# Kernel optimization log

Hardware: AMD Instinct MI355X
Metric: run time of the kernel (lower is better)

## Reference

```python
import jax, jax.numpy as jnp
import numpy as np

N, E = 50000, 600000
IN, H, C = 128, 8, 32
HC = H * C
LAT, OUT, NCOM = 32, 64, 30
BN_EPS = 1e-5
NEG_SLOPE = 0.2


def setup_inputs() -> dict:
    key = jax.random.key(0)
    ks = jax.random.split(key, 32)
    f32 = jnp.float32
    def rn(i, shape, s=0.05):
        return jax.random.normal(ks[i], shape, f32) * s
    inp = {
        'x': jax.random.normal(ks[0], (N, IN), f32),
        'eps': jax.random.normal(ks[1], (N, LAT), f32),
        'edge_index': jax.random.randint(ks[2], (2, E), 0, N, jnp.int32),
        # GAT layer 1 (in -> H*C)
        'gat1_W': rn(3, (IN, HC)), 'gat1_asrc': rn(4, (H, C)), 'gat1_adst': rn(5, (H, C)), 'gat1_b': jnp.zeros((HC,), f32),
        'bn1_g': jnp.ones((HC,), f32), 'bn1_b': jnp.zeros((HC,), f32),
        # GAT layer 2 (H*C -> H*C)
        'gat2_W': rn(6, (HC, HC)), 'gat2_asrc': rn(7, (H, C)), 'gat2_adst': rn(8, (H, C)), 'gat2_b': jnp.zeros((HC,), f32),
        'bn2_g': jnp.ones((HC,), f32), 'bn2_b': jnp.zeros((HC,), f32),
        # GAT layer 3 (H*C -> H*C)
        'gat3_W': rn(9, (HC, HC)), 'gat3_asrc': rn(10, (H, C)), 'gat3_adst': rn(11, (H, C)), 'gat3_b': jnp.zeros((HC,), f32),
        'bn3_g': jnp.ones((HC,), f32), 'bn3_b': jnp.zeros((HC,), f32),
        # heads
        'res_W': rn(12, (IN, HC)), 'res_b': jnp.zeros((HC,), f32),
        'mu_W': rn(13, (HC, LAT)), 'mu_b': jnp.zeros((LAT,), f32),
        'lv_W': rn(14, (HC, LAT)), 'lv_b': jnp.zeros((LAT,), f32),
        'dec_W': rn(15, (LAT, OUT)), 'dec_b': jnp.zeros((OUT,), f32),
        'aux_W': rn(16, (HC, NCOM)), 'aux_b': jnp.zeros((NCOM,), f32),
    }
    return inp


def gat_conv(x, src, dst, W, asrc, adst, b):
    # PyG GATConv (concat=True, self-loops already in src/dst, lin bias=False)
    n = x.shape[0]
    h = (x @ W).reshape(n, H, C)                      # [N,H,C]
    a_s = jnp.einsum('nhc,hc->nh', h, asrc)           # [N,H]
    a_d = jnp.einsum('nhc,hc->nh', h, adst)
    e = jax.nn.leaky_relu(a_s[src] + a_d[dst], NEG_SLOPE)  # [E,H]
    m = jax.ops.segment_max(e, dst, num_segments=n)        # per-dest softmax (stable)
    p = jnp.exp(e - m[dst])
    s = jax.ops.segment_sum(p, dst, num_segments=n)
    alpha = p / (s[dst] + 1e-16)                      # [E,H]
    out = jax.ops.segment_sum(h[src] * alpha[:, :, None], dst, num_segments=n)
    return out.reshape(n, HC) + b


def batch_norm(x, g, b):
    mu = x.mean(0)
    var = x.var(0)  # biased var, as torch BN uses for normalization
    return (x - mu) * jax.lax.rsqrt(var + BN_EPS) * g + b


def reference(x, eps, edge_index,
              gat1_W, gat1_asrc, gat1_adst, gat1_b, bn1_g, bn1_b,
              gat2_W, gat2_asrc, gat2_adst, gat2_b, bn2_g, bn2_b,
              gat3_W, gat3_asrc, gat3_adst, gat3_b, bn3_g, bn3_b,
              res_W, res_b, mu_W, mu_b, lv_W, lv_b, dec_W, dec_b, aux_W, aux_b):
    loops = jnp.arange(N, dtype=edge_index.dtype)
    src = jnp.concatenate([edge_index[0], loops])
    dst = jnp.concatenate([edge_index[1], loops])

    residual = x @ res_W + res_b
    h = jax.nn.relu(batch_norm(gat_conv(x, src, dst, gat1_W, gat1_asrc, gat1_adst, gat1_b), bn1_g, bn1_b))
    h = jax.nn.relu(batch_norm(gat_conv(h, src, dst, gat2_W, gat2_asrc, gat2_adst, gat2_b), bn2_g, bn2_b))
    h = jax.nn.relu(batch_norm(gat_conv(h, src, dst, gat3_W, gat3_asrc, gat3_adst, gat3_b), bn3_g, bn3_b))
    h = h + residual

    mu = h @ mu_W + mu_b
    logvar = h @ lv_W + lv_b
    z = mu + eps * jnp.exp(0.5 * logvar)   # reparameterize
    out = z @ dec_W + dec_b
    aux = h @ aux_W + aux_b
    return (out, mu, logvar, aux)
```

## Files before the change

kernel.cpp:

```cpp
#include <hip/hip_runtime.h>

#define N_NODES 50000
#define N_EDGES 600000
#define HC 256
#define NH 8
#define AGG_BLOCKS 2048
#define AGG_WAVES (AGG_BLOCKS * 4)

typedef short s8v __attribute__((ext_vector_type(8)));
typedef float f4v __attribute__((ext_vector_type(4)));
typedef _Float16 h4v __attribute__((ext_vector_type(4)));
typedef _Float16 h8v __attribute__((ext_vector_type(8)));
typedef __attribute__((address_space(1))) const unsigned int as1_cu32;
typedef __attribute__((address_space(3))) unsigned int as3_u32;

__device__ inline ushort f2bf(float f) {
  unsigned u = __float_as_uint(f);
  unsigned r = u + 0x7FFF + ((u >> 16) & 1);
  return (ushort)(r >> 16);
}

__global__ void k_init_cnt(int* __restrict__ cnt) {
  int i = blockIdx.x * 256 + threadIdx.x;
  if (i < N_NODES) cnt[i] = 1;
}

__global__ void k_count(const int* __restrict__ dstE, int* __restrict__ cnt) {
  int e = blockIdx.x * 256 + threadIdx.x;
  if (e < N_EDGES) atomicAdd(&cnt[dstE[e]], 1);
}

__global__ void k_scan_bsum(const int* __restrict__ cnt, int* __restrict__ bsum) {
  __shared__ int sd[256];
  int i = blockIdx.x * 256 + threadIdx.x;
  sd[threadIdx.x] = (i < N_NODES) ? cnt[i] : 0;
  __syncthreads();
  for (int o = 128; o > 0; o >>= 1) {
    if (threadIdx.x < o) sd[threadIdx.x] += sd[threadIdx.x + o];
    __syncthreads();
  }
  if (threadIdx.x == 0) bsum[blockIdx.x] = sd[0];
}

__global__ void k_scan_offsets(int* __restrict__ bsum, int nb) {
  __shared__ int s[256];
  int t = threadIdx.x;
  int v = (t < nb) ? bsum[t] : 0;
  s[t] = v; __syncthreads();
  for (int o = 1; o < 256; o <<= 1) {
    int x = (t >= o) ? s[t - o] : 0;
    __syncthreads();
    s[t] += x;
    __syncthreads();
  }
  if (t < nb) bsum[t] = s[t] - v;
}

__global__ void k_scan_write(const int* __restrict__ cnt, const int* __restrict__ bsum,
                             int* __restrict__ rowptr, int* __restrict__ fillptr) {
  __shared__ int s[256];
  int t = threadIdx.x;
  int i = blockIdx.x * 256 + t;
  int v = (i < N_NODES) ? cnt[i] : 0;
  s[t] = v; __syncthreads();
  for (int o = 1; o < 256; o <<= 1) {
    int x = (t >= o) ? s[t - o] : 0;
    __syncthreads();
    s[t] += x;
    __syncthreads();
  }
  int excl = s[t] - v + bsum[blockIdx.x];
  if (i < N_NODES) {
    rowptr[i] = excl;
    fillptr[i] = excl;
    if (i == N_NODES - 1) rowptr[N_NODES] = excl + v;
  }
}

__global__ void k_fill(const int* __restrict__ srcE, const int* __restrict__ dstE,
                       int* __restrict__ fillptr, int* __restrict__ srcs) {
  int i = blockIdx.x * 256 + threadIdx.x;
  if (i < N_NODES) {
    int pos = atomicAdd(&fillptr[i], 1);
    srcs[pos] = i;
  } else if (i < N_NODES + N_EDGES) {
    int e = i - N_NODES;
    int pos = atomicAdd(&fillptr[dstE[e]], 1);
    srcs[pos] = srcE[e];
  }
}

__global__ void k_cvt_x(const float* __restrict__ X, ushort* __restrict__ Xb) {
  size_t i = ((size_t)blockIdx.x * 256 + threadIdx.x) * 4;
  float4 x4 = *(const float4*)&X[i];
  ushort4 o;
  o.x = f2bf(x4.x); o.y = f2bf(x4.y); o.z = f2bf(x4.z); o.w = f2bf(x4.w);
  *(ushort4*)&Xb[i] = o;
}

__global__ void k_prep(const float* __restrict__ gW0, const float* __restrict__ resW,
                       const float* __restrict__ gW1, const float* __restrict__ gW2,
                       const float* __restrict__ muW, const float* __restrict__ lvW,
                       const float* __restrict__ auxW,
                       ushort* __restrict__ WtP, ushort* __restrict__ Wt2,
                       ushort* __restrict__ Wt3, ushort* __restrict__ Wth) {
  __shared__ ushort s[32][33];
  int id = blockIdx.x;
  int t = threadIdx.x;
  if (id < 64) {
    const float* W = (id < 32) ? gW0 : resW;
    ushort* Wt = (id < 32) ? WtP : (WtP + 256 * 128);
    int a = id & 31;
    int bx = a & 3, by = a >> 2;
    int tx = t & 31, ty = t >> 5;
    int k0 = bx * 32, n0 = by * 32;
    for (int j = 0; j < 32; j += 8)
      s[ty + j][tx] = f2bf(W[(size_t)(k0 + ty + j) * 256 + n0 + tx]);
    __syncthreads();
    for (int j = 0; j < 32; j += 8)
      Wt[(size_t)(n0 + ty + j) * 128 + k0 + tx] = s[tx][ty + j];
  } else if (id < 192) {
    const float* W = (id < 128) ? gW1 : gW2;
    ushort* Wt = (id < 128) ? Wt2 : Wt3;
    int a = (id - 64) & 63;
    int bx = a & 7, by = a >> 3;
    int tx = t & 31, ty = t >> 5;
    int k0 = bx * 32, n0 = by * 32;
    for (int j = 0; j < 32; j += 8)
      s[ty + j][tx] = f2bf(W[(size_t)(k0 + ty + j) * 256 + n0 + tx]);
    __syncthreads();
    for (int j = 0; j < 32; j += 8)
      Wt[(size_t)(n0 + ty + j) * 256 + k0 + tx] = s[tx][ty + j];
  } else {
    int n = id - 192;
    int k = t;
    float v = 0.f;
    if (n < 32) v = muW[k * 32 + n];
    else if (n < 64) v = lvW[k * 32 + (n - 32)];
    else if (n < 94) v = auxW[k * 30 + (n - 64)];
    Wth[n * 256 + k] = f2bf(v);
  }
}

template <typename OutT>
__launch_bounds__(256)
__global__ void k_gemm_bf16(const ushort* __restrict__ A, const ushort* __restrict__ Wt,
                            const float* __restrict__ bias, int bias_off, OutT* __restrict__ Out,
                            int M, int K, int ldc,
                            const float* __restrict__ att_asrc, const float* __restrict__ att_adst,
                            float* __restrict__ att_as, float* __restrict__ att_ad) {
  __shared__ __align__(16) ushort As[16 * 512];
  __shared__ __align__(16) ushort Bs[8 * 512];
  int t = threadIdx.x, w = t >> 6, L = t & 63;
  int bm = blockIdx.x * 128, bn = blockIdx.y * 64;
  int lrow = L & 15, lcol = (L >> 4) * 8;

  const ushort* ga[4];
  const ushort* gb[2];
#pragma unroll
  for (int u = 0; u < 4; u++) {
    int i = w * 4 + u;
    int mt = i >> 1, ks = i & 1;
    int arow = bm + mt * 16 + lrow;
    if (arow >= M) arow = M - 1;
    ga[u] = A + (size_t)arow * K + ks * 32 + lcol;
  }
#pragma unroll
  for (int u = 0; u < 2; u++) {
    int i = w * 2 + u;
    int mt = i >> 1, ks = i & 1;
    int brow = bn + mt * 16 + lrow;
    gb[u] = Wt + (size_t)brow * K + ks * 32 + lcol;
  }

  f4v acc[4][2];
  f4v zero = {0.f, 0.f, 0.f, 0.f};
#pragma unroll
  for (int mi = 0; mi < 4; mi++)
#pragma unroll
    for (int ni = 0; ni < 2; ni++) acc[mi][ni] = zero;

  int wm = (w >> 1) * 4;
  int wn = (w & 1) * 2;

  int nk = K >> 6;
  for (int kt = 0; kt < nk; kt++) {
#pragma unroll
    for (int u = 0; u < 4; u++) {
      int i = w * 4 + u;
      __builtin_amdgcn_global_load_lds((as1_cu32*)ga[u], (as3_u32*)&As[i * 512], 16, 0, 0);
      ga[u] += 64;
    }
#pragma unroll
    for (int u = 0; u < 2; u++) {
      int i = w * 2 + u;
      __builtin_amdgcn_global_load_lds((as1_cu32*)gb[u], (as3_u32*)&Bs[i * 512], 16, 0, 0);
      gb[u] += 64;
    }
    __syncthreads();
#pragma unroll
    for (int ks = 0; ks < 2; ks++) {
      s8v af[4], bf[2];
#pragma unroll
      for (int mi = 0; mi < 4; mi++)
        af[mi] = *(const s8v*)&As[(((wm + mi) * 2 + ks) * 64 + L) * 8];
#pragma unroll
      for (int ni = 0; ni < 2; ni++)
        bf[ni] = *(const s8v*)&Bs[(((wn + ni) * 2 + ks) * 64 + L) * 8];
#pragma unroll
      for (int mi = 0; mi < 4; mi++)
#pragma unroll
        for (int ni = 0; ni < 2; ni++)
          acc[mi][ni] = __builtin_amdgcn_mfma_f32_16x16x32_bf16(af[mi], bf[ni], acc[mi][ni], 0, 0, 0);
    }
    __syncthreads();
  }
#pragma unroll
  for (int ni = 0; ni < 2; ni++) {
    int col = bn + (wn + ni) * 16 + (L & 15);
    float bb = (bias && col >= bias_off) ? bias[col - bias_off] : 0.f;
#pragma unroll
    for (int mi = 0; mi < 4; mi++) {
      int rbase = bm + (wm + mi) * 16 + (L >> 4) * 4;
#pragma unroll
      for (int i = 0; i < 4; i++) {
        int r = rbase + i;
        if (r < M) Out[(size_t)r * ldc + col] = (OutT)(acc[mi][ni][i] + bb);
      }
    }
  }
  if (att_as && bn < 256) {
    int hb = ((unsigned)(bn + wn * 16)) >> 5;
    int cl = L & 15;
    float sa0 = att_asrc[hb * 32 + cl],  sa1 = att_asrc[hb * 32 + 16 + cl];
    float da0 = att_adst[hb * 32 + cl],  da1 = att_adst[hb * 32 + 16 + cl];
#pragma unroll
    for (int mi = 0; mi < 4; mi++) {
#pragma unroll
      for (int i = 0; i < 4; i++) {
        float vs = acc[mi][0][i] * sa0 + acc[mi][1][i] * sa1;
        float vd = acc[mi][0][i] * da0 + acc[mi][1][i] * da1;
        vs += __shfl_xor(vs, 1); vd += __shfl_xor(vd, 1);
        vs += __shfl_xor(vs, 2); vd += __shfl_xor(vd, 2);
        vs += __shfl_xor(vs, 4); vd += __shfl_xor(vd, 4);
        vs += __shfl_xor(vs, 8); vd += __shfl_xor(vd, 8);
        int r = bm + (wm + mi) * 16 + (L >> 4) * 4 + i;
        if (cl == 0 && r < M) {
          att_as[r * NH + hb] = vs;
          att_ad[r * NH + hb] = vd;
        }
      }
    }
  }
}

__launch_bounds__(256)
__global__ void k_gemm_head(const ushort* __restrict__ A, const ushort* __restrict__ Wt,
                            const float* __restrict__ eps,
                            const float* __restrict__ mub, const float* __restrict__ lvb,
                            const float* __restrict__ auxb,
                            const float* __restrict__ decW, const float* __restrict__ decb,
                            float* __restrict__ out) {
  __shared__ __align__(16) ushort smem[16384];
  __shared__ float wsd[2048];
  __shared__ float shz[4][32];
  ushort* As = smem;
  ushort* Bs = smem + 8192;
  int t = threadIdx.x, w = t >> 6, L = t & 63;
  int bm = blockIdx.x * 128;
  int lrow = L & 15, lcol = (L >> 4) * 8;
  const int K = 256;
  for (int i = t; i < 2048; i += 256) wsd[i] = decW[i];

  const ushort* ga[4];
  const ushort* gb[4];
#pragma unroll
  for (int u = 0; u < 4; u++) {
    int i = w * 4 + u;
    int mt = i >> 1, ks = i & 1;
    int arow = bm + mt * 16 + lrow;
    if (arow >= N_NODES) arow = N_NODES - 1;
    ga[u] = A + (size_t)arow * K + ks * 32 + lcol;
    int brow = mt * 16 + lrow;
    gb[u] = Wt + (size_t)brow * K + ks * 32 + lcol;
  }
  f4v acc[4][4];
  f4v zero = {0.f, 0.f, 0.f, 0.f};
#pragma unroll
  for (int mi = 0; mi < 4; mi++)
#pragma unroll
    for (int ni = 0; ni < 4; ni++) acc[mi][ni] = zero;
  int wm = (w >> 1) * 4;
  int wn = (w & 1) * 4;
  for (int kt = 0; kt < 4; kt++) {
#pragma unroll
    for (int u = 0; u < 4; u++) {
      int i = w * 4 + u;
      __builtin_amdgcn_global_load_lds((as1_cu32*)ga[u], (as3_u32*)&As[i * 512], 16, 0, 0);
      __builtin_amdgcn_global_load_lds((as1_cu32*)gb[u], (as3_u32*)&Bs[i * 512], 16, 0, 0);
      ga[u] += 64; gb[u] += 64;
    }
    __syncthreads();
#pragma unroll
    for (int ks = 0; ks < 2; ks++) {
      s8v af[4], bf[4];
#pragma unroll
      for (int mi = 0; mi < 4; mi++)
        af[mi] = *(const s8v*)&As[(((wm + mi) * 2 + ks) * 64 + L) * 8];
#pragma unroll
      for (int ni = 0; ni < 4; ni++)
        bf[ni] = *(const s8v*)&Bs[(((wn + ni) * 2 + ks) * 64 + L) * 8];
#pragma unroll
      for (int mi = 0; mi < 4; mi++)
#pragma unroll
        for (int ni = 0; ni < 4; ni++)
          acc[mi][ni] = __builtin_amdgcn_mfma_f32_16x16x32_bf16(af[mi], bf[ni], acc[mi][ni], 0, 0, 0);
    }
    __syncthreads();
  }
  _Float16* tile = (_Float16*)smem;
#pragma unroll
  for (int ni = 0; ni < 4; ni++) {
    int c = (wn + ni) * 16 + (L & 15);
#pragma unroll
    for (int mi = 0; mi < 4; mi++) {
      int rbase = (wm + mi) * 16 + (L >> 4) * 4;
#pragma unroll
      for (int i = 0; i < 4; i++)
        tile[(rbase + i) * 128 + c] = (_Float16)acc[mi][ni][i];
    }
  }
  __syncthreads();
  for (int rr = 0; rr < 32; rr++) {
    int rl = w * 32 + rr;
    int n = bm + rl;
    bool valid = n < N_NODES;
    if (L < 32) {
      float mu = (float)tile[rl * 128 + L] + mub[L];
      float lv = (float)tile[rl * 128 + 32 + L] + lvb[L];
      float zv = 0.f;
      if (valid) {
        out[(size_t)N_NODES * 64 + (size_t)n * 32 + L] = mu;
        out[(size_t)N_NODES * 96 + (size_t)n * 32 + L] = lv;
        zv = mu + eps[(size_t)n * 32 + L] * __expf(0.5f * lv);
      }
      shz[w][L] = zv;
    } else if (L < 62 && valid) {
      int j = L - 32;
      out[(size_t)N_NODES * 128 + (size_t)n * 30 + j] = (float)tile[rl * 128 + 64 + j] + auxb[j];
    }
    __syncthreads();
    float o = decb[L];
#pragma unroll 8
    for (int kk = 0; kk < 32; kk++) o += shz[w][kk] * wsd[kk * 64 + L];
    if (valid) out[(size_t)n * 64 + L] = o;
    __syncthreads();
  }
}

#define FMA4(P, B2)                                                                        \
  asm("v_fma_mix_f32 %0, %1, %2, %0 op_sel:[0,0,0] op_sel_hi:[0,1,0]"                      \
      : "+v"(ac0) : "v"(P), "v"((B2).x));                                                  \
  asm("v_fma_mix_f32 %0, %1, %2, %0 op_sel:[0,1,0] op_sel_hi:[0,1,0]"                      \
      : "+v"(ac1) : "v"(P), "v"((B2).x));                                                  \
  asm("v_fma_mix_f32 %0, %1, %2, %0 op_sel:[0,0,0] op_sel_hi:[0,1,0]"                      \
      : "+v"(ac2) : "v"(P), "v"((B2).y));                                                  \
  asm("v_fma_mix_f32 %0, %1, %2, %0 op_sel:[0,1,0] op_sel_hi:[0,1,0]"                      \
      : "+v"(ac3) : "v"(P), "v"((B2).y));

__launch_bounds__(256)
__global__ void k_agg(const int* __restrict__ rowptr, const int* __restrict__ srcs,
                      const float* __restrict__ as_, const float* __restrict__ ad_,
                      const _Float16* __restrict__ B, int ld, const float* __restrict__ gb,
                      _Float16* __restrict__ C, float* __restrict__ part,
                      float* __restrict__ stats) {
  __shared__ float ss[4 * 512];
  int t = threadIdx.x;
  if (blockIdx.x == 0) {
    stats[t] = 0.f; stats[t + 256] = 0.f;
  }
  int w = t >> 6, lane = t & 63;
  int h = lane >> 3;
  int cb = lane << 2;
  int ldu = ld >> 2;
  const uint2* Bu = (const uint2*)B;
  float4 g4 = *(const float4*)&gb[cb];
  float sts0 = 0.f, sts1 = 0.f, sts2 = 0.f, sts3 = 0.f;
  float stq0 = 0.f, stq1 = 0.f, stq2 = 0.f, stq3 = 0.f;

  for (int n = blockIdx.x * 4 + w; n < N_NODES; n += AGG_WAVES) {
    int beg = rowptr[n], end = rowptr[n + 1];
    float ad_nh = ad_[n * NH + h];
    float ac0 = 0.f, ac1 = 0.f, ac2 = 0.f, ac3 = 0.f, wsum = 0.f;
    int k = beg;
    for (; k + 4 <= end; k += 4) {
      int s0 = srcs[k], s1 = srcs[k + 1], s2 = srcs[k + 2], s3 = srcs[k + 3];
      uint2 b0 = Bu[(size_t)s0 * ldu + lane];
      uint2 b1 = Bu[(size_t)s1 * ldu + lane];
      uint2 b2 = Bu[(size_t)s2 * ldu + lane];
      uint2 b3 = Bu[(size_t)s3 * ldu + lane];
      float e0 = as_[s0 * NH + h] + ad_nh; e0 = e0 > 0.f ? e0 : 0.2f * e0;
      float e1 = as_[s1 * NH + h] + ad_nh; e1 = e1 > 0.f ? e1 : 0.2f * e1;
      float e2 = as_[s2 * NH + h] + ad_nh; e2 = e2 > 0.f ? e2 : 0.2f * e2;
      float e3 = as_[s3 * NH + h] + ad_nh; e3 = e3 > 0.f ? e3 : 0.2f * e3;
      float p0 = __expf(e0), p1 = __expf(e1), p2 = __expf(e2), p3 = __expf(e3);
      wsum += (p0 + p1) + (p2 + p3);
      FMA4(p0, b0)
      FMA4(p1, b1)
      FMA4(p2, b2)
      FMA4(p3, b3)
    }
    for (; k < end; k++) {
      int s = srcs[k];
      h4v b4 = *(const h4v*)&B[(size_t)s * ld + cb];
      float e = as_[s * NH + h] + ad_nh;
      e = e > 0.f ? e : 0.2f * e;
      float p = __expf(e);
      wsum += p;
      ac0 += p * (float)b4[0]; ac1 += p * (float)b4[1];
      ac2 += p * (float)b4[2]; ac3 += p * (float)b4[3];
    }
    float inv = 1.f / (wsum + 1e-16f);
    float v0 = ac0 * inv + g4.x, v1 = ac1 * inv + g4.y;
    float v2 = ac2 * inv + g4.z, v3 = ac3 * inv + g4.w;
    h4v o; o[0] = (_Float16)v0; o[1] = (_Float16)v1; o[2] = (_Float16)v2; o[3] = (_Float16)v3;
    *(h4v*)&C[(size_t)n * 256 + cb] = o;
    sts0 += v0; stq0 += v0 * v0;
    sts1 += v1; stq1 += v1 * v1;
    sts2 += v2; stq2 += v2 * v2;
    sts3 += v3; stq3 += v3 * v3;
  }
  float* sw = &ss[w * 512];
  sw[cb + 0] = sts0; sw[cb + 1] = sts1; sw[cb + 2] = sts2; sw[cb + 3] = sts3;
  sw[256 + cb + 0] = stq0; sw[256 + cb + 1] = stq1;
  sw[256 + cb + 2] = stq2; sw[256 + cb + 3] = stq3;
  __syncthreads();
  float p0 = ss[t] + ss[512 + t] + ss[1024 + t] + ss[1536 + t];
  float p1 = ss[256 + t] + ss[768 + t] + ss[1280 + t] + ss[1792 + t];
  part[(size_t)blockIdx.x * 512 + t] = p0;
  part[(size_t)blockIdx.x * 512 + 256 + t] = p1;
}

__global__ void k_bn_reduce(const float* __restrict__ part, float* __restrict__ stats) {
  int i = threadIdx.x;
  int base = blockIdx.x * (AGG_BLOCKS / 16);
  float s0 = 0.f, s1 = 0.f;
  for (int b = 0; b < AGG_BLOCKS / 16; b++) {
    s0 += part[(size_t)(base + b) * 512 + i];
    s1 += part[(size_t)(base + b) * 512 + 256 + i];
  }
  atomicAdd(&stats[i], s0);
  atomicAdd(&stats[256 + i], s1);
}

__global__ void k_bn_relu_cvt(const _Float16* __restrict__ X, const float* __restrict__ stats,
                              const float* __restrict__ g, const float* __restrict__ b,
                              const _Float16* __restrict__ resid, int rld,
                              ushort* __restrict__ Xb) {
  size_t i = ((size_t)blockIdx.x * 256 + threadIdx.x) * 8;
  int c = (int)(i & 255);
  const float invN = 1.f / (float)N_NODES;
  h8v x8 = *(const h8v*)&X[i];
  float v[8];
#pragma unroll
  for (int q = 0; q < 2; q++) {
    float4 s4 = *(const float4*)&stats[c + q * 4];
    float4 q4 = *(const float4*)&stats[256 + c + q * 4];
    float4 g4 = *(const float4*)&g[c + q * 4];
    float4 b4 = *(const float4*)&b[c + q * 4];
    float m0 = s4.x * invN, m1 = s4.y * invN, m2 = s4.z * invN, m3 = s4.w * invN;
    v[q * 4 + 0] = ((float)x8[q * 4 + 0] - m0) * rsqrtf(q4.x * invN - m0 * m0 + 1e-5f) * g4.x + b4.x;
    v[q * 4 + 1] = ((float)x8[q * 4 + 1] - m1) * rsqrtf(q4.y * invN - m1 * m1 + 1e-5f) * g4.y + b4.y;
    v[q * 4 + 2] = ((float)x8[q * 4 + 2] - m2) * rsqrtf(q4.z * invN - m2 * m2 + 1e-5f) * g4.z + b4.z;
    v[q * 4 + 3] = ((float)x8[q * 4 + 3] - m3) * rsqrtf(q4.w * invN - m3 * m3 + 1e-5f) * g4.w + b4.w;
  }
#pragma unroll
  for (int q = 0; q < 8; q++) v[q] = v[q] > 0.f ? v[q] : 0.f;
  if (resid) {
    size_t row = i >> 8;
    h8v r8 = *(const h8v*)&resid[row * rld + c];
#pragma unroll
    for (int q = 0; q < 8; q++) v[q] += (float)r8[q];
  }
  ushort o8[8];
#pragma unroll
  for (int q = 0; q < 8; q++) o8[q] = f2bf(v[q]);
  *(uint4*)&Xb[i] = *(const uint4*)o8;
}

extern "C" void kernel_launch(void* const* d_in, const int* in_sizes, int n_in,
                              void* d_out, int out_size, void* d_ws, size_t ws_size,
                              hipStream_t stream) {
  (void)in_sizes; (void)n_in; (void)out_size; (void)ws_size;
  const float* x    = (const float*)d_in[0];
  const float* eps  = (const float*)d_in[1];
  const int*   ei   = (const int*)d_in[2];
  const float* gW[3]    = {(const float*)d_in[3],  (const float*)d_in[9],  (const float*)d_in[15]};
  const float* gasrc[3] = {(const float*)d_in[4],  (const float*)d_in[10], (const float*)d_in[16]};
  const float* gadst[3] = {(const float*)d_in[5],  (const float*)d_in[11], (const float*)d_in[17]};
  const float* gbias[3] = {(const float*)d_in[6],  (const float*)d_in[12], (const float*)d_in[18]};
  const float* bng[3]   = {(const float*)d_in[7],  (const float*)d_in[13], (const float*)d_in[19]};
  const float* bnb[3]   = {(const float*)d_in[8],  (const float*)d_in[14], (const float*)d_in[20]};
  const float* resW = (const float*)d_in[21];
  const float* resb = (const float*)d_in[22];
  const float* muW  = (const float*)d_in[23];
  const float* mub  = (const float*)d_in[24];
  const float* lvW  = (const float*)d_in[25];
  const float* lvb  = (const float*)d_in[26];
  const float* decW = (const float*)d_in[27];
  const float* decb = (const float*)d_in[28];
  const float* auxW = (const float*)d_in[29];
  const float* auxb = (const float*)d_in[30];
  float* out = (float*)d_out;

  char* ws = (char*)d_ws;
  size_t off = 0;
  auto alloc = [&](size_t bytes) -> void* {
    void* p = ws + off;
    off += (bytes + 255) & ~(size_t)255;
    return p;
  };
  _Float16* X0R = (_Float16*)alloc((size_t)N_NODES * 512 * 2);
  _Float16* X0  = (_Float16*)alloc((size_t)N_NODES * HC * 2);
  _Float16* X1  = (_Float16*)alloc((size_t)N_NODES * HC * 2);
  ushort* Xb    = (ushort*)alloc((size_t)N_NODES * HC * 2);
  float*  as_   = (float*)alloc((size_t)N_NODES * NH * 4);
  float*  ad_   = (float*)alloc((size_t)N_NODES * NH * 4);
  float*  stats = (float*)alloc(512 * 4);
  float*  part  = (float*)alloc((size_t)AGG_BLOCKS * 512 * 4);
  int* cnt      = (int*)alloc((size_t)N_NODES * 4);
  int* rowptr   = (int*)alloc((size_t)(N_NODES + 1) * 4);
  int* fillptr  = (int*)alloc((size_t)N_NODES * 4);
  int* srcs     = (int*)alloc((size_t)(N_NODES + N_EDGES) * 4);
  int* bsum     = (int*)alloc(256 * 4);
  ushort* WtP   = (ushort*)alloc(512 * 128 * 2);
  ushort* Wt2   = (ushort*)alloc(256 * 256 * 2);
  ushort* Wt3   = (ushort*)alloc(256 * 256 * 2);
  ushort* Wth   = (ushort*)alloc(128 * 256 * 2);

  const int NB = (N_NODES + 255) / 256;
  k_init_cnt<<<NB, 256, 0, stream>>>(cnt);
  k_count<<<(N_EDGES + 255) / 256, 256, 0, stream>>>(ei + N_EDGES, cnt);
  k_scan_bsum<<<NB, 256, 0, stream>>>(cnt, bsum);
  k_scan_offsets<<<1, 256, 0, stream>>>(bsum, NB);
  k_scan_write<<<NB, 256, 0, stream>>>(cnt, bsum, rowptr, fillptr);
  k_fill<<<(N_NODES + N_EDGES + 255) / 256, 256, 0, stream>>>(ei, ei + N_EDGES, fillptr, srcs);

  k_prep<<<320, 256, 0, stream>>>(gW[0], resW, gW[1], gW[2], muW, lvW, auxW, WtP, Wt2, Wt3, Wth);
  k_cvt_x<<<(N_NODES * 128) / 1024, 256, 0, stream>>>(x, Xb);

  const int GM = (N_NODES + 127) / 128;
  const int EW_GRID = (N_NODES * HC) / 2048;

  k_gemm_bf16<_Float16><<<dim3(GM, 8), 256, 0, stream>>>(
      Xb, WtP, resb, 256, X0R, N_NODES, 128, 512, gasrc[0], gadst[0], as_, ad_);
  k_agg<<<AGG_BLOCKS, 256, 0, stream>>>(rowptr, srcs, as_, ad_, X0R, 512, gbias[0], X1, part, stats);
  k_bn_reduce<<<16, 256, 0, stream>>>(part, stats);
  k_bn_relu_cvt<<<EW_GRID, 256, 0, stream>>>(X1, stats, bng[0], bnb[0], nullptr, 0, Xb);

  const ushort* Wts[2] = {Wt2, Wt3};
  for (int L = 0; L < 2; L++) {
    k_gemm_bf16<_Float16><<<dim3(GM, 4), 256, 0, stream>>>(
        Xb, Wts[L], nullptr, 0, X0, N_NODES, 256, 256, gasrc[L + 1], gadst[L + 1], as_, ad_);
    k_agg<<<AGG_BLOCKS, 256, 0, stream>>>(rowptr, srcs, as_, ad_, X0, 256, gbias[L + 1], X1, part, stats);
    k_bn_reduce<<<16, 256, 0, stream>>>(part, stats);
    k_bn_relu_cvt<<<EW_GRID, 256, 0, stream>>>(
        X1, stats, bng[L + 1], bnb[L + 1], (L == 1) ? (X0R + 256) : nullptr, 512, Xb);
  }
  k_gemm_head<<<GM, 256, 0, stream>>>(Xb, Wth, eps, mub, lvb, auxb, decW, decb, out);
}
```

Before: 608.2 us.

## Fuse batch-norm, ReLU and residual into next GEMM's A-tile load

Removes the standalone BN+ReLU+bf16 conversion kernel by applying normalization, ReLU and (for the final layer) residual addition while staging the A tile in the following GEMM and head kernels. This avoids a full write and re-read of the intermediate activation buffer and several launches. In exchange, A tiles are loaded synchronously through registers instead of via async global-to-LDS copies, and each row is re-normalized once per column block of the GEMM grid.

```diff
diff --git a/kernel.cpp b/kernel.cpp
--- a/kernel.cpp
+++ b/kernel.cpp
@@ -255,7 +255,140 @@
 }
 
 __launch_bounds__(256)
-__global__ void k_gemm_head(const ushort* __restrict__ A, const ushort* __restrict__ Wt,
+__global__ void k_gemm_bn(const _Float16* __restrict__ A, const ushort* __restrict__ Wt,
+                          const float* __restrict__ stats, const float* __restrict__ g,
+                          const float* __restrict__ b, _Float16* __restrict__ Out,
+                          const float* __restrict__ att_asrc, const float* __restrict__ att_adst,
+                          float* __restrict__ att_as, float* __restrict__ att_ad) {
+  __shared__ __align__(16) ushort As[16 * 512];
+  __shared__ __align__(16) ushort Bs[8 * 512];
+  const int K = 256, M = N_NODES, ldc = 256;
+  const float invN = 1.f / (float)N_NODES;
+  int t = threadIdx.x, w = t >> 6, L = t & 63;
+  int bm = blockIdx.x * 128, bn = blockIdx.y * 64;
+  int lrow = L & 15, lcol = (L >> 4) * 8;
+
+  int arow[4];
+  const ushort* gb[2];
+#pragma unroll
+  for (int u = 0; u < 4; u++) {
+    int i = w * 4 + u;
+    int mt = i >> 1;
+    int r = bm + mt * 16 + lrow;
+    arow[u] = (r >= M) ? (M - 1) : r;
+  }
+#pragma unroll
+  for (int u = 0; u < 2; u++) {
+    int i = w * 2 + u;
+    int mt = i >> 1, ks = i & 1;
+    gb[u] = Wt + (size_t)(bn + mt * 16 + lrow) * K + ks * 32 + lcol;
+  }
+
+  f4v acc[4][2];
+  f4v zero = {0.f, 0.f, 0.f, 0.f};
+#pragma unroll
+  for (int mi = 0; mi < 4; mi++)
+#pragma unroll
+    for (int ni = 0; ni < 2; ni++) acc[mi][ni] = zero;
+
+  int wm = (w >> 1) * 4;
+  int wn = (w & 1) * 2;
+
+  for (int kt = 0; kt < 4; kt++) {
+#pragma unroll
+    for (int u = 0; u < 2; u++) {
+      int i = w * 2 + u;
+      __builtin_amdgcn_global_load_lds((as1_cu32*)gb[u], (as3_u32*)&Bs[i * 512], 16, 0, 0);
+      gb[u] += 64;
+    }
+#pragma unroll
+    for (int u = 0; u < 4; u++) {
+      int i = w * 4 + u;
+      int ks = i & 1;
+      int c0 = kt * 64 + ks * 32 + lcol;
+      h8v a8 = *(const h8v*)&A[(size_t)arow[u] * 256 + c0];
+      ushort o8[8];
+#pragma unroll
+      for (int q2 = 0; q2 < 2; q2++) {
+        float4 s4 = *(const float4*)&stats[c0 + q2 * 4];
+        float4 q4 = *(const float4*)&stats[256 + c0 + q2 * 4];
+        float4 g4 = *(const float4*)&g[c0 + q2 * 4];
+        float4 b4 = *(const float4*)&b[c0 + q2 * 4];
+        float sm[4] = {s4.x, s4.y, s4.z, s4.w};
+        float qm[4] = {q4.x, q4.y, q4.z, q4.w};
+        float gm[4] = {g4.x, g4.y, g4.z, g4.w};
+        float bm_[4] = {b4.x, b4.y, b4.z, b4.w};
+#pragma unroll
+        for (int j = 0; j < 4; j++) {
+          float m = sm[j] * invN;
+          float rs = rsqrtf(qm[j] * invN - m * m + 1e-5f) * gm[j];
+          float v = ((float)a8[q2 * 4 + j] - m) * rs + bm_[j];
+          v = v > 0.f ? v : 0.f;
+          o8[q2 * 4 + j] = f2bf(v);
+        }
+      }
+      *(uint4*)&As[(size_t)i * 512 + L * 8] = *(const uint4*)o8;
+    }
+    __syncthreads();
+#pragma unroll
+    for (int ks = 0; ks < 2; ks++) {
+      s8v af[4], bf[2];
+#pragma unroll
+      for (int mi = 0; mi < 4; mi++)
+        af[mi] = *(const s8v*)&As[(((wm + mi) * 2 + ks) * 64 + L) * 8];
+#pragma unroll
+      for (int ni = 0; ni < 2; ni++)
+        bf[ni] = *(const s8v*)&Bs[(((wn + ni) * 2 + ks) * 64 + L) * 8];
+#pragma unroll
+      for (int mi = 0; mi < 4; mi++)
+#pragma unroll
+        for (int ni = 0; ni < 2; ni++)
+          acc[mi][ni] = __builtin_amdgcn_mfma_f32_16x16x32_bf16(af[mi], bf[ni], acc[mi][ni], 0, 0, 0);
+    }
+    __syncthreads();
+  }
+#pragma unroll
+  for (int ni = 0; ni < 2; ni++) {
+    int col = bn + (wn + ni) * 16 + (L & 15);
+#pragma unroll
+    for (int mi = 0; mi < 4; mi++) {
+      int rbase = bm + (wm + mi) * 16 + (L >> 4) * 4;
+#pragma unroll
+      for (int i = 0; i < 4; i++) {
+        int r = rbase + i;
+        if (r < M) Out[(size_t)r * ldc + col] = (_Float16)(acc[mi][ni][i]);
+      }
+    }
+  }
+  {
+    int hb = ((unsigned)(bn + wn * 16)) >> 5;
+    int cl = L & 15;
+    float sa0 = att_asrc[hb * 32 + cl],  sa1 = att_asrc[hb * 32 + 16 + cl];
+    float da0 = att_adst[hb * 32 + cl],  da1 = att_adst[hb * 32 + 16 + cl];
+#pragma unroll
+    for (int mi = 0; mi < 4; mi++) {
+#pragma unroll
+      for (int i = 0; i < 4; i++) {
+        float vs = acc[mi][0][i] * sa0 + acc[mi][1][i] * sa1;
+        float vd = acc[mi][0][i] * da0 + acc[mi][1][i] * da1;
+        vs += __shfl_xor(vs, 1); vd += __shfl_xor(vd, 1);
+        vs += __shfl_xor(vs, 2); vd += __shfl_xor(vd, 2);
+        vs += __shfl_xor(vs, 4); vd += __shfl_xor(vd, 4);
+        vs += __shfl_xor(vs, 8); vd += __shfl_xor(vd, 8);
+        int r = bm + (wm + mi) * 16 + (L >> 4) * 4 + i;
+        if (cl == 0 && r < M) {
+          att_as[r * NH + hb] = vs;
+          att_ad[r * NH + hb] = vd;
+        }
+      }
+    }
+  }
+}
+
+__launch_bounds__(256)
+__global__ void k_gemm_head(const _Float16* __restrict__ A, const _Float16* __restrict__ resid,
+                            const float* __restrict__ stats, const float* __restrict__ g,
+                            const float* __restrict__ b, const ushort* __restrict__ Wt,
                             const float* __restrict__ eps,
                             const float* __restrict__ mub, const float* __restrict__ lvb,
                             const float* __restrict__ auxb,
@@ -266,21 +399,21 @@
   __shared__ float shz[4][32];
   ushort* As = smem;
   ushort* Bs = smem + 8192;
+  const float invN = 1.f / (float)N_NODES;
   int t = threadIdx.x, w = t >> 6, L = t & 63;
   int bm = blockIdx.x * 128;
   int lrow = L & 15, lcol = (L >> 4) * 8;
   const int K = 256;
   for (int i = t; i < 2048; i += 256) wsd[i] = decW[i];
 
-  const ushort* ga[4];
+  int arow[4];
   const ushort* gb[4];
 #pragma unroll
   for (int u = 0; u < 4; u++) {
     int i = w * 4 + u;
     int mt = i >> 1, ks = i & 1;
-    int arow = bm + mt * 16 + lrow;
-    if (arow >= N_NODES) arow = N_NODES - 1;
-    ga[u] = A + (size_t)arow * K + ks * 32 + lcol;
+    int r = bm + mt * 16 + lrow;
+    arow[u] = (r >= N_NODES) ? (N_NODES - 1) : r;
     int brow = mt * 16 + lrow;
     gb[u] = Wt + (size_t)brow * K + ks * 32 + lcol;
   }
@@ -296,9 +429,38 @@
 #pragma unroll
     for (int u = 0; u < 4; u++) {
       int i = w * 4 + u;
-      __builtin_amdgcn_global_load_lds((as1_cu32*)ga[u], (as3_u32*)&As[i * 512], 16, 0, 0);
       __builtin_amdgcn_global_load_lds((as1_cu32*)gb[u], (as3_u32*)&Bs[i * 512], 16, 0, 0);
-      ga[u] += 64; gb[u] += 64;
+      gb[u] += 64;
+    }
+#pragma unroll
+    for (int u = 0; u < 4; u++) {
+      int i = w * 4 + u;
+      int ks = i & 1;
+      int c0 = kt * 64 + ks * 32 + lcol;
+      h8v a8 = *(const h8v*)&A[(size_t)arow[u] * 256 + c0];
+      h8v r8 = *(const h8v*)&resid[(size_t)arow[u] * 512 + c0];
+      ushort o8[8];
+#pragma unroll
+      for (int q2 = 0; q2 < 2; q2++) {
+        float4 s4 = *(const float4*)&stats[c0 + q2 * 4];
+        float4 q4 = *(const float4*)&stats[256 + c0 + q2 * 4];
+        float4 g4 = *(const float4*)&g[c0 + q2 * 4];
+        float4 b4 = *(const float4*)&b[c0 + q2 * 4];
+        float sm[4] = {s4.x, s4.y, s4.z, s4.w};
+        float qm[4] = {q4.x, q4.y, q4.z, q4.w};
+        float gm[4] = {g4.x, g4.y, g4.z, g4.w};
+        float bm_[4] = {b4.x, b4.y, b4.z, b4.w};
+#pragma unroll
+        for (int j = 0; j < 4; j++) {
+          float m = sm[j] * invN;
+          float rs = rsqrtf(qm[j] * invN - m * m + 1e-5f) * gm[j];
+          float v = ((float)a8[q2 * 4 + j] - m) * rs + bm_[j];
+          v = v > 0.f ? v : 0.f;
+          v += (float)r8[q2 * 4 + j];
+          o8[q2 * 4 + j] = f2bf(v);
+        }
+      }
+      *(uint4*)&As[(size_t)i * 512 + L * 8] = *(const uint4*)o8;
     }
     __syncthreads();
 #pragma unroll
@@ -451,41 +613,6 @@
   }
   atomicAdd(&stats[i], s0);
   atomicAdd(&stats[256 + i], s1);
-}
-
-__global__ void k_bn_relu_cvt(const _Float16* __restrict__ X, const float* __restrict__ stats,
-                              const float* __restrict__ g, const float* __restrict__ b,
-                              const _Float16* __restrict__ resid, int rld,
-                              ushort* __restrict__ Xb) {
-  size_t i = ((size_t)blockIdx.x * 256 + threadIdx.x) * 8;
-  int c = (int)(i & 255);
-  const float invN = 1.f / (float)N_NODES;
-  h8v x8 = *(const h8v*)&X[i];
-  float v[8];
-#pragma unroll
-  for (int q = 0; q < 2; q++) {
-    float4 s4 = *(const float4*)&stats[c + q * 4];
-    float4 q4 = *(const float4*)&stats[256 + c + q * 4];
-    float4 g4 = *(const float4*)&g[c + q * 4];
-    float4 b4 = *(const float4*)&b[c + q * 4];
-    float m0 = s4.x * invN, m1 = s4.y * invN, m2 = s4.z * invN, m3 = s4.w * invN;
-    v[q * 4 + 0] = ((float)x8[q * 4 + 0] - m0) * rsqrtf(q4.x * invN - m0 * m0 + 1e-5f) * g4.x + b4.x;
-    v[q * 4 + 1] = ((float)x8[q * 4 + 1] - m1) * rsqrtf(q4.y * invN - m1 * m1 + 1e-5f) * g4.y + b4.y;
-    v[q * 4 + 2] = ((float)x8[q * 4 + 2] - m2) * rsqrtf(q4.z * invN - m2 * m2 + 1e-5f) * g4.z + b4.z;
-    v[q * 4 + 3] = ((float)x8[q * 4 + 3] - m3) * rsqrtf(q4.w * invN - m3 * m3 + 1e-5f) * g4.w + b4.w;
-  }
-#pragma unroll
-  for (int q = 0; q < 8; q++) v[q] = v[q] > 0.f ? v[q] : 0.f;
-  if (resid) {
-    size_t row = i >> 8;
-    h8v r8 = *(const h8v*)&resid[row * rld + c];
-#pragma unroll
-    for (int q = 0; q < 8; q++) v[q] += (float)r8[q];
-  }
-  ushort o8[8];
-#pragma unroll
-  for (int q = 0; q < 8; q++) o8[q] = f2bf(v[q]);
-  *(uint4*)&Xb[i] = *(const uint4*)o8;
 }
 
 extern "C" void kernel_launch(void* const* d_in, const int* in_sizes, int n_in,
@@ -550,22 +677,22 @@
   k_cvt_x<<<(N_NODES * 128) / 1024, 256, 0, stream>>>(x, Xb);
 
   const int GM = (N_NODES + 127) / 128;
-  const int EW_GRID = (N_NODES * HC) / 2048;
 
   k_gemm_bf16<_Float16><<<dim3(GM, 8), 256, 0, stream>>>(
       Xb, WtP, resb, 256, X0R, N_NODES, 128, 512, gasrc[0], gadst[0], as_, ad_);
   k_agg<<<AGG_BLOCKS, 256, 0, stream>>>(rowptr, srcs, as_, ad_, X0R, 512, gbias[0], X1, part, stats);
   k_bn_reduce<<<16, 256, 0, stream>>>(part, stats);
-  k_bn_relu_cvt<<<EW_GRID, 256, 0, stream>>>(X1, stats, bng[0], bnb[0], nullptr, 0, Xb);
-
-  const ushort* Wts[2] = {Wt2, Wt3};
-  for (int L = 0; L < 2; L++) {
-    k_gemm_bf16<_Float16><<<dim3(GM, 4), 256, 0, stream>>>(
-        Xb, Wts[L], nullptr, 0, X0, N_NODES, 256, 256, gasrc[L + 1], gadst[L + 1], as_, ad_);
-    k_agg<<<AGG_BLOCKS, 256, 0, stream>>>(rowptr, srcs, as_, ad_, X0, 256, gbias[L + 1], X1, part, stats);
-    k_bn_reduce<<<16, 256, 0, stream>>>(part, stats);
-    k_bn_relu_cvt<<<EW_GRID, 256, 0, stream>>>(
-        X1, stats, bng[L + 1], bnb[L + 1], (L == 1) ? (X0R + 256) : nullptr, 512, Xb);
-  }
-  k_gemm_head<<<GM, 256, 0, stream>>>(Xb, Wth, eps, mub, lvb, auxb, decW, decb, out);
-}
+
+  k_gemm_bn<<<dim3(GM, 4), 256, 0, stream>>>(
+      X1, Wt2, stats, bng[0], bnb[0], X0, gasrc[1], gadst[1], as_, ad_);
+  k_agg<<<AGG_BLOCKS, 256, 0, stream>>>(rowptr, srcs, as_, ad_, X0, 256, gbias[1], X1, part, stats);
+  k_bn_reduce<<<16, 256, 0, stream>>>(part, stats);
+
+  k_gemm_bn<<<dim3(GM, 4), 256, 0, stream>>>(
+      X1, Wt3, stats, bng[1], bnb[1], X0, gasrc[2], gadst[2], as_, ad_);
+  k_agg<<<AGG_BLOCKS, 256, 0, stream>>>(rowptr, srcs, as_, ad_, X0, 256, gbias[2], X1, part, stats);
+  k_bn_reduce<<<16, 256, 0, stream>>>(part, stats);
+
+  k_gemm_head<<<GM, 256, 0, stream>>>(
+      X1, X0R + 256, stats, bng[2], bnb[2], Wth, eps, mub, lvb, auxb, decW, decb, out);
+}
```

After: 664.2 us. 9.2% more time.

## Split GAT aggregation per head across blocks with edge-parallel lanes

Applied to the files above, without the earlier changes.

The aggregation kernel now assigns one attention head per block and has each wave process four edges at once, with 16 lanes per edge each covering two channels, followed by a cross-lane shuffle reduction. This aims to shrink the per-block gathered feature footprint and to better parallelise nodes with short edge lists. In exchange, index and attention-score loads repeat once per head, lanes are partially idle on tails and stores, and the loads are narrower. The BN statistics reduction is reorganised to per-head partials written directly, removing the atomics and the zeroing step.

```diff
diff --git a/kernel.cpp b/kernel.cpp
--- a/kernel.cpp
+++ b/kernel.cpp
@@ -5,7 +5,6 @@
 #define HC 256
 #define NH 8
 #define AGG_BLOCKS 2048
-#define AGG_WAVES (AGG_BLOCKS * 4)
 
 typedef short s8v __attribute__((ext_vector_type(8)));
 typedef float f4v __attribute__((ext_vector_type(4)));
@@ -358,99 +357,74 @@
   }
 }
 
-#define FMA4(P, B2)                                                                        \
-  asm("v_fma_mix_f32 %0, %1, %2, %0 op_sel:[0,0,0] op_sel_hi:[0,1,0]"                      \
-      : "+v"(ac0) : "v"(P), "v"((B2).x));                                                  \
-  asm("v_fma_mix_f32 %0, %1, %2, %0 op_sel:[0,1,0] op_sel_hi:[0,1,0]"                      \
-      : "+v"(ac1) : "v"(P), "v"((B2).x));                                                  \
-  asm("v_fma_mix_f32 %0, %1, %2, %0 op_sel:[0,0,0] op_sel_hi:[0,1,0]"                      \
-      : "+v"(ac2) : "v"(P), "v"((B2).y));                                                  \
-  asm("v_fma_mix_f32 %0, %1, %2, %0 op_sel:[0,1,0] op_sel_hi:[0,1,0]"                      \
-      : "+v"(ac3) : "v"(P), "v"((B2).y));
-
 __launch_bounds__(256)
 __global__ void k_agg(const int* __restrict__ rowptr, const int* __restrict__ srcs,
                       const float* __restrict__ as_, const float* __restrict__ ad_,
                       const _Float16* __restrict__ B, int ld, const float* __restrict__ gb,
-                      _Float16* __restrict__ C, float* __restrict__ part,
-                      float* __restrict__ stats) {
-  __shared__ float ss[4 * 512];
+                      _Float16* __restrict__ C, float* __restrict__ part) {
+  __shared__ float ss[4 * 64];
   int t = threadIdx.x;
-  if (blockIdx.x == 0) {
-    stats[t] = 0.f; stats[t + 256] = 0.f;
-  }
   int w = t >> 6, lane = t & 63;
-  int h = lane >> 3;
-  int cb = lane << 2;
-  int ldu = ld >> 2;
-  const uint2* Bu = (const uint2*)B;
-  float4 g4 = *(const float4*)&gb[cb];
-  float sts0 = 0.f, sts1 = 0.f, sts2 = 0.f, sts3 = 0.f;
-  float stq0 = 0.f, stq1 = 0.f, stq2 = 0.f, stq3 = 0.f;
-
-  for (int n = blockIdx.x * 4 + w; n < N_NODES; n += AGG_WAVES) {
+  int h = blockIdx.x & 7;
+  int q = lane & 15;
+  int j = lane >> 4;
+  int c = h * 32 + q * 2;
+  float gb0 = gb[c], gb1 = gb[c + 1];
+  float sts0 = 0.f, sts1 = 0.f, stq0 = 0.f, stq1 = 0.f;
+
+  for (int n = (blockIdx.x >> 3) * 4 + w; n < N_NODES; n += 1024) {
     int beg = rowptr[n], end = rowptr[n + 1];
     float ad_nh = ad_[n * NH + h];
-    float ac0 = 0.f, ac1 = 0.f, ac2 = 0.f, ac3 = 0.f, wsum = 0.f;
-    int k = beg;
-    for (; k + 4 <= end; k += 4) {
-      int s0 = srcs[k], s1 = srcs[k + 1], s2 = srcs[k + 2], s3 = srcs[k + 3];
-      uint2 b0 = Bu[(size_t)s0 * ldu + lane];
-      uint2 b1 = Bu[(size_t)s1 * ldu + lane];
-      uint2 b2 = Bu[(size_t)s2 * ldu + lane];
-      uint2 b3 = Bu[(size_t)s3 * ldu + lane];
-      float e0 = as_[s0 * NH + h] + ad_nh; e0 = e0 > 0.f ? e0 : 0.2f * e0;
-      float e1 = as_[s1 * NH + h] + ad_nh; e1 = e1 > 0.f ? e1 : 0.2f * e1;
-      float e2 = as_[s2 * NH + h] + ad_nh; e2 = e2 > 0.f ? e2 : 0.2f * e2;
-      float e3 = as_[s3 * NH + h] + ad_nh; e3 = e3 > 0.f ? e3 : 0.2f * e3;
-      float p0 = __expf(e0), p1 = __expf(e1), p2 = __expf(e2), p3 = __expf(e3);
-      wsum += (p0 + p1) + (p2 + p3);
-      FMA4(p0, b0)
-      FMA4(p1, b1)
-      FMA4(p2, b2)
-      FMA4(p3, b3)
-    }
-    for (; k < end; k++) {
-      int s = srcs[k];
-      h4v b4 = *(const h4v*)&B[(size_t)s * ld + cb];
+    float ac0 = 0.f, ac1 = 0.f, wsum = 0.f;
+    for (int k = beg; k < end; k += 4) {
+      int idx = k + j;
+      bool valid = idx < end;
+      if (!valid) idx = end - 1;
+      int s = srcs[idx];
       float e = as_[s * NH + h] + ad_nh;
       e = e > 0.f ? e : 0.2f * e;
-      float p = __expf(e);
+      float p = valid ? __expf(e) : 0.f;
+      uint b2 = *(const uint*)&B[(size_t)s * ld + c];
       wsum += p;
-      ac0 += p * (float)b4[0]; ac1 += p * (float)b4[1];
-      ac2 += p * (float)b4[2]; ac3 += p * (float)b4[3];
-    }
+      asm("v_fma_mix_f32 %0, %1, %2, %0 op_sel:[0,0,0] op_sel_hi:[0,1,0]"
+          : "+v"(ac0) : "v"(p), "v"(b2));
+      asm("v_fma_mix_f32 %0, %1, %2, %0 op_sel:[0,1,0] op_sel_hi:[0,1,0]"
+          : "+v"(ac1) : "v"(p), "v"(b2));
+    }
+    ac0 += __shfl_xor(ac0, 16);  ac0 += __shfl_xor(ac0, 32);
+    ac1 += __shfl_xor(ac1, 16);  ac1 += __shfl_xor(ac1, 32);
+    wsum += __shfl_xor(wsum, 16); wsum += __shfl_xor(wsum, 32);
     float inv = 1.f / (wsum + 1e-16f);
-    float v0 = ac0 * inv + g4.x, v1 = ac1 * inv + g4.y;
-    float v2 = ac2 * inv + g4.z, v3 = ac3 * inv + g4.w;
-    h4v o; o[0] = (_Float16)v0; o[1] = (_Float16)v1; o[2] = (_Float16)v2; o[3] = (_Float16)v3;
-    *(h4v*)&C[(size_t)n * 256 + cb] = o;
-    sts0 += v0; stq0 += v0 * v0;
-    sts1 += v1; stq1 += v1 * v1;
-    sts2 += v2; stq2 += v2 * v2;
-    sts3 += v3; stq3 += v3 * v3;
-  }
-  float* sw = &ss[w * 512];
-  sw[cb + 0] = sts0; sw[cb + 1] = sts1; sw[cb + 2] = sts2; sw[cb + 3] = sts3;
-  sw[256 + cb + 0] = stq0; sw[256 + cb + 1] = stq1;
-  sw[256 + cb + 2] = stq2; sw[256 + cb + 3] = stq3;
+    float v0 = ac0 * inv + gb0, v1 = ac1 * inv + gb1;
+    if (lane < 16) {
+      _Float16 o2[2] = {(_Float16)v0, (_Float16)v1};
+      *(uint*)&C[(size_t)n * 256 + c] = *(const uint*)o2;
+      sts0 += v0; stq0 += v0 * v0;
+      sts1 += v1; stq1 += v1 * v1;
+    }
+  }
+  if (lane < 16) {
+    ss[w * 64 + q * 2]          = sts0;
+    ss[w * 64 + q * 2 + 1]      = sts1;
+    ss[w * 64 + 32 + q * 2]     = stq0;
+    ss[w * 64 + 32 + q * 2 + 1] = stq1;
+  }
   __syncthreads();
-  float p0 = ss[t] + ss[512 + t] + ss[1024 + t] + ss[1536 + t];
-  float p1 = ss[256 + t] + ss[768 + t] + ss[1280 + t] + ss[1792 + t];
-  part[(size_t)blockIdx.x * 512 + t] = p0;
-  part[(size_t)blockIdx.x * 512 + 256 + t] = p1;
+  if (t < 64) {
+    float p0 = ss[t] + ss[64 + t] + ss[128 + t] + ss[192 + t];
+    part[(size_t)blockIdx.x * 64 + t] = p0;
+  }
 }
 
 __global__ void k_bn_reduce(const float* __restrict__ part, float* __restrict__ stats) {
-  int i = threadIdx.x;
-  int base = blockIdx.x * (AGG_BLOCKS / 16);
-  float s0 = 0.f, s1 = 0.f;
-  for (int b = 0; b < AGG_BLOCKS / 16; b++) {
-    s0 += part[(size_t)(base + b) * 512 + i];
-    s1 += part[(size_t)(base + b) * 512 + 256 + i];
-  }
-  atomicAdd(&stats[i], s0);
-  atomicAdd(&stats[256 + i], s1);
+  int e = blockIdx.x * 256 + threadIdx.x;
+  int kind = e >> 8;
+  int c = e & 255;
+  int g = c >> 5, ci = c & 31;
+  float s = 0.f;
+  for (int jb = 0; jb < AGG_BLOCKS / 8; jb++)
+    s += part[(size_t)(jb * 8 + g) * 64 + kind * 32 + ci];
+  stats[e] = s;
 }
 
 __global__ void k_bn_relu_cvt(const _Float16* __restrict__ X, const float* __restrict__ stats,
@@ -527,7 +501,7 @@
   float*  as_   = (float*)alloc((size_t)N_NODES * NH * 4);
   float*  ad_   = (float*)alloc((size_t)N_NODES * NH * 4);
   float*  stats = (float*)alloc(512 * 4);
-  float*  part  = (float*)alloc((size_t)AGG_BLOCKS * 512 * 4);
+  float*  part  = (float*)alloc((size_t)AGG_BLOCKS * 64 * 4);
   int* cnt      = (int*)alloc((size_t)N_NODES * 4);
   int* rowptr   = (int*)alloc((size_t)(N_NODES + 1) * 4);
   int* fillptr  = (int*)alloc((size_t)N_NODES * 4);
@@ -554,16 +528,16 @@
 
   k_gemm_bf16<_Float16><<<dim3(GM, 8), 256, 0, stream>>>(
       Xb, WtP, resb, 256, X0R, N_NODES, 128, 512, gasrc[0], gadst[0], as_, ad_);
-  k_agg<<<AGG_BLOCKS, 256, 0, stream>>>(rowptr, srcs, as_, ad_, X0R, 512, gbias[0], X1, part, stats);
-  k_bn_reduce<<<16, 256, 0, stream>>>(part, stats);
+  k_agg<<<AGG_BLOCKS, 256, 0, stream>>>(rowptr, srcs, as_, ad_, X0R, 512, gbias[0], X1, part);
+  k_bn_reduce<<<2, 256, 0, stream>>>(part, stats);
   k_bn_relu_cvt<<<EW_GRID, 256, 0, stream>>>(X1, stats, bng[0], bnb[0], nullptr, 0, Xb);
 
   const ushort* Wts[2] = {Wt2, Wt3};
   for (int L = 0; L < 2; L++) {
     k_gemm_bf16<_Float16><<<dim3(GM, 4), 256, 0, stream>>>(
         Xb, Wts[L], nullptr, 0, X0, N_NODES, 256, 256, gasrc[L + 1], gadst[L + 1], as_, ad_);
-    k_agg<<<AGG_BLOCKS, 256, 0, stream>>>(rowptr, srcs, as_, ad_, X0, 256, gbias[L + 1], X1, part, stats);
-    k_bn_reduce<<<16, 256, 0, stream>>>(part, stats);
+    k_agg<<<AGG_BLOCKS, 256, 0, stream>>>(rowptr, srcs, as_, ad_, X0, 256, gbias[L + 1], X1, part);
+    k_bn_reduce<<<2, 256, 0, stream>>>(part, stats);
     k_bn_relu_cvt<<<EW_GRID, 256, 0, stream>>>(
         X1, stats, bng[L + 1], bnb[L + 1], (L == 1) ? (X0R + 256) : nullptr, 512, Xb);
   }
```

Measured after the change: 1.066 ms. 75.2% more time.

## Preload full weight tile to LDS and read A fragments directly from global

Applied to the files above, without the earlier changes.

The bf16 GEMM now templates K, loads the whole B (weight) panel for the block into LDS once, and streams A fragments straight from global memory into registers instead of staging them through LDS per k-step. This removes the per-iteration barriers and the A staging, aiming to cut synchronisation and LDS traffic in the node-feature projection GEMMs. It raises LDS use (up to 32KB for K=256), which may limit occupancy. A rows are read from global by each wave without sharing, which could increase global or cache traffic.

```diff
diff --git a/kernel.cpp b/kernel.cpp
--- a/kernel.cpp
+++ b/kernel.cpp
@@ -142,35 +142,36 @@
   }
 }
 
-template <typename OutT>
+template <int K, typename OutT>
 __launch_bounds__(256)
 __global__ void k_gemm_bf16(const ushort* __restrict__ A, const ushort* __restrict__ Wt,
                             const float* __restrict__ bias, int bias_off, OutT* __restrict__ Out,
-                            int M, int K, int ldc,
+                            int M, int ldc,
                             const float* __restrict__ att_asrc, const float* __restrict__ att_adst,
                             float* __restrict__ att_as, float* __restrict__ att_ad) {
-  __shared__ __align__(16) ushort As[16 * 512];
-  __shared__ __align__(16) ushort Bs[8 * 512];
+  constexpr int S = K / 32;
+  __shared__ __align__(16) ushort Bs[4 * S * 512];
   int t = threadIdx.x, w = t >> 6, L = t & 63;
   int bm = blockIdx.x * 128, bn = blockIdx.y * 64;
   int lrow = L & 15, lcol = (L >> 4) * 8;
 
-  const ushort* ga[4];
-  const ushort* gb[2];
-#pragma unroll
-  for (int u = 0; u < 4; u++) {
-    int i = w * 4 + u;
-    int mt = i >> 1, ks = i & 1;
-    int arow = bm + mt * 16 + lrow;
-    if (arow >= M) arow = M - 1;
-    ga[u] = A + (size_t)arow * K + ks * 32 + lcol;
-  }
-#pragma unroll
-  for (int u = 0; u < 2; u++) {
-    int i = w * 2 + u;
-    int mt = i >> 1, ks = i & 1;
-    int brow = bn + mt * 16 + lrow;
-    gb[u] = Wt + (size_t)brow * K + ks * 32 + lcol;
+  {
+    const ushort* gsrc = Wt + (size_t)(bn + w * 16 + lrow) * K + lcol;
+#pragma unroll
+    for (int s = 0; s < S; s++) {
+      __builtin_amdgcn_global_load_lds((as1_cu32*)(gsrc + s * 32),
+                                       (as3_u32*)&Bs[(w * S + s) * 512], 16, 0, 0);
+    }
+  }
+
+  const ushort* pa[4];
+  int wm = (w >> 1) * 4;
+  int wn = (w & 1) * 2;
+#pragma unroll
+  for (int mi = 0; mi < 4; mi++) {
+    int r = bm + (wm + mi) * 16 + lrow;
+    if (r >= M) r = M - 1;
+    pa[mi] = A + (size_t)r * K + lcol;
   }
 
   f4v acc[4][2];
@@ -180,41 +181,24 @@
 #pragma unroll
     for (int ni = 0; ni < 2; ni++) acc[mi][ni] = zero;
 
-  int wm = (w >> 1) * 4;
-  int wn = (w & 1) * 2;
-
-  int nk = K >> 6;
-  for (int kt = 0; kt < nk; kt++) {
-#pragma unroll
-    for (int u = 0; u < 4; u++) {
-      int i = w * 4 + u;
-      __builtin_amdgcn_global_load_lds((as1_cu32*)ga[u], (as3_u32*)&As[i * 512], 16, 0, 0);
-      ga[u] += 64;
-    }
-#pragma unroll
-    for (int u = 0; u < 2; u++) {
-      int i = w * 2 + u;
-      __builtin_amdgcn_global_load_lds((as1_cu32*)gb[u], (as3_u32*)&Bs[i * 512], 16, 0, 0);
-      gb[u] += 64;
-    }
-    __syncthreads();
-#pragma unroll
-    for (int ks = 0; ks < 2; ks++) {
-      s8v af[4], bf[2];
-#pragma unroll
-      for (int mi = 0; mi < 4; mi++)
-        af[mi] = *(const s8v*)&As[(((wm + mi) * 2 + ks) * 64 + L) * 8];
+  __syncthreads();
+
+#pragma unroll
+  for (int s = 0; s < S; s++) {
+    s8v af[4], bf[2];
+#pragma unroll
+    for (int mi = 0; mi < 4; mi++)
+      af[mi] = *(const s8v*)(pa[mi] + s * 32);
+#pragma unroll
+    for (int ni = 0; ni < 2; ni++)
+      bf[ni] = *(const s8v*)&Bs[(((wn + ni) * S + s) * 64 + L) * 8];
+#pragma unroll
+    for (int mi = 0; mi < 4; mi++)
 #pragma unroll
       for (int ni = 0; ni < 2; ni++)
-        bf[ni] = *(const s8v*)&Bs[(((wn + ni) * 2 + ks) * 64 + L) * 8];
-#pragma unroll
-      for (int mi = 0; mi < 4; mi++)
-#pragma unroll
-        for (int ni = 0; ni < 2; ni++)
-          acc[mi][ni] = __builtin_amdgcn_mfma_f32_16x16x32_bf16(af[mi], bf[ni], acc[mi][ni], 0, 0, 0);
-    }
-    __syncthreads();
-  }
+        acc[mi][ni] = __builtin_amdgcn_mfma_f32_16x16x32_bf16(af[mi], bf[ni], acc[mi][ni], 0, 0, 0);
+  }
+
 #pragma unroll
   for (int ni = 0; ni < 2; ni++) {
     int col = bn + (wn + ni) * 16 + (L & 15);
@@ -552,16 +536,16 @@
   const int GM = (N_NODES + 127) / 128;
   const int EW_GRID = (N_NODES * HC) / 2048;
 
-  k_gemm_bf16<_Float16><<<dim3(GM, 8), 256, 0, stream>>>(
-      Xb, WtP, resb, 256, X0R, N_NODES, 128, 512, gasrc[0], gadst[0], as_, ad_);
+  k_gemm_bf16<128, _Float16><<<dim3(GM, 8), 256, 0, stream>>>(
+      Xb, WtP, resb, 256, X0R, N_NODES, 512, gasrc[0], gadst[0], as_, ad_);
   k_agg<<<AGG_BLOCKS, 256, 0, stream>>>(rowptr, srcs, as_, ad_, X0R, 512, gbias[0], X1, part, stats);
   k_bn_reduce<<<16, 256, 0, stream>>>(part, stats);
   k_bn_relu_cvt<<<EW_GRID, 256, 0, stream>>>(X1, stats, bng[0], bnb[0], nullptr, 0, Xb);
 
   const ushort* Wts[2] = {Wt2, Wt3};
   for (int L = 0; L < 2; L++) {
-    k_gemm_bf16<_Float16><<<dim3(GM, 4), 256, 0, stream>>>(
-        Xb, Wts[L], nullptr, 0, X0, N_NODES, 256, 256, gasrc[L + 1], gadst[L + 1], as_, ad_);
+    k_gemm_bf16<256, _Float16><<<dim3(GM, 4), 256, 0, stream>>>(
+        Xb, Wts[L], nullptr, 0, X0, N_NODES, 256, gasrc[L + 1], gadst[L + 1], as_, ad_);
     k_agg<<<AGG_BLOCKS, 256, 0, stream>>>(rowptr, srcs, as_, ad_, X0, 256, gbias[L + 1], X1, part, stats);
     k_bn_reduce<<<16, 256, 0, stream>>>(part, stats);
     k_bn_relu_cvt<<<EW_GRID, 256, 0, stream>>>(
```

New measurement: 633.9 us. +4.2%, slower.
